# Optimization experiments

Hardware: AMD Instinct MI355X
Metric: run time of the kernel (lower is better)

The kernel has to match this reference:

```python
import jax, jax.numpy as jnp
import numpy as np

D_MODEL = 768
STATE_N = 16
BATCH = 8
SEQ = 2048


def setup_inputs() -> dict:
    key = jax.random.key(0)
    ks = jax.random.split(key, 12)
    d, n = D_MODEL, STATE_N
    s = 0.02
    inp = {
        "x": jax.random.normal(ks[0], (BATCH, SEQ, d), dtype=jnp.float32),
        # A_log init as in module: log(arange(1..N)) repeated over d_model
        "A_log": jnp.log(jnp.tile(jnp.arange(1, n + 1, dtype=jnp.float32)[None, :], (d, 1))),
        "D_param": jnp.ones((d,), dtype=jnp.float32),
        "B_proj_w": jax.random.normal(ks[1], (n, d), dtype=jnp.float32) * s,
        "C_proj_w": jax.random.normal(ks[2], (n, d), dtype=jnp.float32) * s,
        "delta_w": jax.random.normal(ks[3], (d, d), dtype=jnp.float32) * s,
        "delta_b": jax.random.normal(ks[4], (d,), dtype=jnp.float32) * s,
        "in_w": jax.random.normal(ks[5], (2 * d, d), dtype=jnp.float32) * s,
        "in_b": jax.random.normal(ks[6], (2 * d,), dtype=jnp.float32) * s,
        "out_w": jax.random.normal(ks[7], (d, d), dtype=jnp.float32) * s,
        "out_b": jax.random.normal(ks[8], (d,), dtype=jnp.float32) * s,
        "conv_w": jax.random.normal(ks[9], (d, 1, 3), dtype=jnp.float32) * s,  # depthwise [D,1,K]
        "conv_b": jax.random.normal(ks[10], (d,), dtype=jnp.float32) * s,
    }
    return inp


def _forward(x, A_log, D_param, B_proj_w, C_proj_w, delta_w, delta_b,
             in_w, in_b, out_w, out_b, conv_w, conv_b):
    A = -jnp.exp(A_log)  # [D, N]
    xz = jnp.einsum("bld,ed->ble", x, in_w) + in_b  # [B, L, 2D]
    x_in, z = jnp.split(xz, 2, axis=-1)
    # depthwise conv1d, padding=1, groups=D (cross-correlation, same as torch)
    x_c = jax.lax.conv_general_dilated(
        jnp.transpose(x_in, (0, 2, 1)), conv_w,
        window_strides=(1,), padding=((1, 1),),
        feature_group_count=x.shape[-1],
        dimension_numbers=("NCH", "OIH", "NCH"))
    x_conv = jnp.transpose(x_c, (0, 2, 1)) + conv_b  # [B, L, D]
    x_conv = jax.nn.silu(x_conv)
    delta = jax.nn.softplus(jnp.einsum("bld,ed->ble", x_conv, delta_w) + delta_b)  # [B,L,D]
    B_sel = jnp.einsum("bld,nd->bln", x_conv, B_proj_w)  # [B, L, N]
    C_sel = jnp.einsum("bld,nd->bln", x_conv, C_proj_w)  # [B, L, N]

    Bsz, L, D = x.shape
    N = A.shape[1]

    def step(h, t_in):
        dt, b_t, c_t, x_t = t_in  # [B,D], [B,N], [B,N], [B,D]
        A_bar = jnp.exp(dt[:, :, None] * A[None, :, :])           # [B,D,N]
        h = A_bar * h + (dt[:, :, None] * b_t[:, None, :]) * x_t[:, :, None]
        y_t = jnp.sum(h * c_t[:, None, :], axis=-1)               # [B,D]
        return h, y_t

    xs = (jnp.transpose(delta, (1, 0, 2)), jnp.transpose(B_sel, (1, 0, 2)),
          jnp.transpose(C_sel, (1, 0, 2)), jnp.transpose(x_conv, (1, 0, 2)))
    h0 = jnp.zeros((Bsz, D, N), dtype=x.dtype)
    _, ys = jax.lax.scan(step, h0, xs)
    y = jnp.transpose(ys, (1, 0, 2))  # [B, L, D]

    y = y + x_conv * D_param[None, None, :]
    y = y * jax.nn.silu(z)
    return jnp.einsum("bld,ed->ble", y, out_w) + out_b


def reference(x, A_log, D_param, B_proj_w, C_proj_w, delta_w, delta_b,
              in_w, in_b, out_w, out_b, conv_w, conv_b):
    return _forward(x, A_log, D_param, B_proj_w, C_proj_w, delta_w, delta_b,
                    in_w, in_b, out_w, out_b, conv_w, conv_b)
```

## Files before the change

### kernel.cpp

```cpp
#include <hip/hip_runtime.h>
#include <hip/hip_bf16.h>

#define D_MODEL 768
#define SEQL    2048
#define BATCH   8
#define NSTATE  16
#define NCHUNK  32
#define TCHUNK  64

typedef __attribute__((ext_vector_type(8))) short short8;
typedef __attribute__((ext_vector_type(4))) float f32x4;

typedef const __attribute__((address_space(1))) unsigned int gas1_t;
typedef __attribute__((address_space(3))) unsigned int las3_t;

__device__ __forceinline__ void gload_lds16(const void* g, void* l) {
  __builtin_amdgcn_global_load_lds((gas1_t*)g, (las3_t*)l, 16, 0, 0);
}

__device__ __forceinline__ float b2f(short s) {
  return __uint_as_float(((unsigned)(unsigned short)s) << 16);
}
__device__ __forceinline__ short f2b(float f) {
  __hip_bfloat16 h = __float2bfloat16(f);
  return *reinterpret_cast<short*>(&h);
}

__device__ __forceinline__ unsigned tix(int r, int k) {
  return (unsigned)((((r >> 7) * 24 + (k >> 5)) << 13) + ((r & 127) << 6) +
                    ((((k >> 3) ^ ((r >> 1) & 3)) & 3) << 4) + ((k & 7) << 1));
}

__device__ __forceinline__ short8 pack8(const float* v) {
  short8 o;
#pragma unroll
  for (int e = 0; e < 8; ++e) o[e] = f2b(v[e]);
  return o;
}

__global__ __launch_bounds__(256) void prep_all(
    const float* __restrict__ x, const float* __restrict__ in_w,
    const float* __restrict__ delta_w, const float* __restrict__ Bp,
    const float* __restrict__ Cp, const float* __restrict__ out_w,
    const float* __restrict__ A_log,
    char* __restrict__ xb, char* __restrict__ w_in,
    char* __restrict__ w_dbc, char* __restrict__ w_out,
    float* __restrict__ A2) {
  int i = blockIdx.x * 256 + threadIdx.x;
  if (i < 16384 * 96) {
    const int r = i / 96, k8 = i - r * 96;
    float v[8];
    *(float4*)(v) = *(const float4*)(x + (size_t)r * 768 + k8 * 8);
    *(float4*)(v + 4) = *(const float4*)(x + (size_t)r * 768 + k8 * 8 + 4);
    *(short8*)(xb + tix(r, k8 * 8)) = pack8(v);
    return;
  }
  i -= 16384 * 96;
  if (i < 1536 * 96) {
    const int r = i / 96, k8 = i - r * 96;
    float v[8];
    *(float4*)(v) = *(const float4*)(in_w + (size_t)r * 768 + k8 * 8);
    *(float4*)(v + 4) = *(const float4*)(in_w + (size_t)r * 768 + k8 * 8 + 4);
    *(short8*)(w_in + tix(r, k8 * 8)) = pack8(v);
    return;
  }
  i -= 1536 * 96;
  if (i < 896 * 96) {
    const int r = i / 96, k8 = i - r * 96;
    float v[8];
    const float* src = (r < 768)   ? delta_w + (size_t)r * 768
                       : (r < 784) ? Bp + (size_t)(r - 768) * 768
                       : (r < 800) ? Cp + (size_t)(r - 784) * 768
                                   : nullptr;
    if (src) {
      *(float4*)(v) = *(const float4*)(src + k8 * 8);
      *(float4*)(v + 4) = *(const float4*)(src + k8 * 8 + 4);
    } else {
#pragma unroll
      for (int e = 0; e < 8; ++e) v[e] = 0.f;
    }
    *(short8*)(w_dbc + tix(r, k8 * 8)) = pack8(v);
    return;
  }
  i -= 896 * 96;
  if (i < 768 * 96) {
    const int r = i / 96, k8 = i - r * 96;
    float v[8];
    *(float4*)(v) = *(const float4*)(out_w + (size_t)r * 768 + k8 * 8);
    *(float4*)(v + 4) = *(const float4*)(out_w + (size_t)r * 768 + k8 * 8 + 4);
    *(short8*)(w_out + tix(r, k8 * 8)) = pack8(v);
    return;
  }
  i -= 768 * 96;
  A2[i] = -expf(A_log[i]) * 1.44269504088896f;
}

template <int MODE>
__global__ __launch_bounds__(256, 3) void gemm128tb(
    const char* __restrict__ Amat, const char* __restrict__ Bw,
    const float* __restrict__ bias, void* __restrict__ out0,
    void* __restrict__ out1, void* __restrict__ out2, const int gxn) {
  constexpr int KT = 24;
  __shared__ char lds[49152];
  const int tid  = threadIdx.x;
  const int lane = tid & 63, wave = tid >> 6;
  const int wr = wave >> 1, wc = wave & 1;

  const int nwg = gridDim.x, id = blockIdx.x;
  const int swz = (id & 7) * (nwg >> 3) + (id >> 3);
  const int tm = swz / gxn, tn = swz - tm * gxn;

  const char* gA = Amat + ((size_t)tm * KT) * 8192 + (tid << 4);
  const char* gB = Bw   + ((size_t)tn * KT) * 8192 + (tid << 4);
  const int ldst = tid << 4;

  const int frow = lane & 15, fq = lane >> 4;
  const int pc = (fq << 4) ^ (((frow >> 1) & 3) << 4);
  const int aoff = ((wr * 64 + frow) << 6) + pc;
  const int boff = ((wc * 64 + frow) << 6) + pc;

  f32x4 acc[4][4];
#pragma unroll
  for (int m = 0; m < 4; ++m)
#pragma unroll
    for (int n = 0; n < 4; ++n) acc[m][n] = (f32x4){0.f, 0.f, 0.f, 0.f};

#define STAGE(buf, kt)                                                          \
  {                                                                             \
    const char* sA = gA + (kt) * 8192;                                          \
    const char* sB = gB + (kt) * 8192;                                          \
    char* dA = lds + (buf) * 16384 + ldst;                                      \
    char* dB = dA + 8192;                                                       \
    gload_lds16(sA, dA);                                                        \
    gload_lds16(sA + 4096, dA + 4096);                                          \
    gload_lds16(sB, dB);                                                        \
    gload_lds16(sB + 4096, dB + 4096);                                          \
  }
#define VMW(n) asm volatile("s_waitcnt vmcnt(" #n ")" ::: "memory")
#define BAR    __builtin_amdgcn_s_barrier()

  STAGE(0, 0);
  STAGE(1, 1);
  VMW(4);
  BAR;

  int bc = 0;
  for (int kt = 0; kt < KT; ++kt) {
    short8 a[4], b[4];
    const char* ba = lds + bc * 16384;
#pragma unroll
    for (int m = 0; m < 4; ++m) a[m] = *(const short8*)(ba + aoff + m * 1024);
#pragma unroll
    for (int n = 0; n < 4; ++n) b[n] = *(const short8*)(ba + 8192 + boff + n * 1024);
    const bool st = (kt + 2 < KT);
    if (st) {
      const int b2 = bc + 2 >= 3 ? bc - 1 : bc + 2;
      STAGE(b2, kt + 2);
    }
    __builtin_amdgcn_s_setprio(1);
#pragma unroll
    for (int m = 0; m < 4; ++m)
#pragma unroll
      for (int n = 0; n < 4; ++n)
        acc[m][n] = __builtin_amdgcn_mfma_f32_16x16x32_bf16(a[m], b[n], acc[m][n], 0, 0, 0);
    __builtin_amdgcn_s_setprio(0);
    if (st)                VMW(4);
    else if (kt + 2 == KT) VMW(0);
    BAR;
    bc = bc + 1 >= 3 ? 0 : bc + 1;
  }

  const int rowA0 = tm * 128, rowB0 = tn * 128;
#pragma unroll
  for (int m = 0; m < 4; ++m) {
    const int grow0 = rowA0 + wr * 64 + m * 16 + fq * 4;
#pragma unroll
    for (int n = 0; n < 4; ++n) {
      const int gcol = rowB0 + wc * 64 + n * 16 + frow;
#pragma unroll
      for (int i = 0; i < 4; ++i) {
        const int grow = grow0 + i;
        float v = acc[m][n][i];
        if (MODE == 0) {
          v += bias[gcol];
          if (gcol < 768)
            *(short*)((char*)out0 + tix(grow, gcol)) = f2b(v);
          else
            *(short*)((char*)out1 + tix(grow, gcol - 768)) = f2b(v);
        } else if (MODE == 1) {
          if (gcol < 768) {
            v += bias[gcol];
            float sp = (v > 20.f) ? v : log1pf(expf(v));
            *(short*)((char*)out0 + tix(grow, gcol)) = f2b(sp);
          } else if (gcol < 784) {
            ((float*)out1)[(size_t)grow * 16 + (gcol - 768)] = v;
          } else if (gcol < 800) {
            ((float*)out2)[(size_t)grow * 16 + (gcol - 784)] = v;
          }
        } else {
          ((float*)out0)[(size_t)grow * 768 + gcol] = v + bias[gcol];
        }
      }
    }
  }
#undef STAGE
#undef VMW
#undef BAR
}

__global__ __launch_bounds__(256) void conv_silu8(
    const char* __restrict__ xin, const float* __restrict__ conv_w,
    const float* __restrict__ conv_b, char* __restrict__ xc) {
  const int idx = blockIdx.x * 256 + threadIdx.x;
  const int r  = idx / 96;
  const int d8 = (idx - r * 96) * 8;
  const int t  = r & (SEQL - 1);

  short8 x0 = *(const short8*)(xin + tix(r, d8));
  short8 xm = {}, xp = {};
  if (t > 0)        xm = *(const short8*)(xin + tix(r - 1, d8));
  if (t < SEQL - 1) xp = *(const short8*)(xin + tix(r + 1, d8));

  const float4* cw4 = (const float4*)(conv_w + d8 * 3);
  float4 cw[6];
#pragma unroll
  for (int q = 0; q < 6; ++q) cw[q] = cw4[q];
  float4 cb0 = *(const float4*)(conv_b + d8);
  float4 cb1 = *(const float4*)(conv_b + d8 + 4);
  const float* cwf = (const float*)cw;
  const float* cbf0 = (const float*)&cb0;
  const float* cbf1 = (const float*)&cb1;

  short8 res;
#pragma unroll
  for (int e = 0; e < 8; ++e) {
    float acc = (e < 4) ? cbf0[e] : cbf1[e - 4];
    acc = fmaf(cwf[e * 3 + 0], b2f(xm[e]), acc);
    acc = fmaf(cwf[e * 3 + 1], b2f(x0[e]), acc);
    acc = fmaf(cwf[e * 3 + 2], b2f(xp[e]), acc);
    const float sig = 1.f / (1.f + __expf(-acc));
    res[e] = f2b(acc * sig);
  }
  *(short8*)(xc + tix(r, d8)) = res;
}

__global__ __launch_bounds__(256) void scan_pass1(
    const char* __restrict__ delta, const char* __restrict__ xconv,
    const float* __restrict__ Bsel, const float* __restrict__ A2,
    float* __restrict__ sumdt, float* __restrict__ Sbuf) {
  const int d = blockIdx.x * 256 + threadIdx.x;
  const int b = blockIdx.y, c = blockIdx.z;
  __shared__ float sB[TCHUNK * 16];
  ((float4*)sB)[threadIdx.x] =
      ((const float4*)(Bsel + ((size_t)b * SEQL + c * TCHUNK) * 16))[threadIdx.x];
  __syncthreads();

  float a2[16];
#pragma unroll
  for (int n = 0; n < 16; ++n) a2[n] = A2[d * 16 + n];
  float h[16] = {};
  float sdt = 0.f;
  const int r0 = b * SEQL + c * TCHUNK;
  const unsigned tb = (((unsigned)((r0 >> 7) * 24 + (d >> 5))) << 13) + ((r0 & 127) << 6);
  const unsigned sd0 = (d >> 3) & 3;
  const unsigned klo = (d & 7) << 1;
  for (int t = 0; t < TCHUNK; ++t) {
    const unsigned ro = tb + t * 64 + (((sd0 ^ ((unsigned)t >> 1)) & 3) << 4) + klo;
    const float dt = b2f(*(const short*)(delta + ro));
    const float x = b2f(*(const short*)(xconv + ro));
    sdt += dt;
    const float dtx = dt * x;
    const float* Br = &sB[t * 16];
#pragma unroll
    for (int n = 0; n < 16; ++n) {
      const float a = exp2f(dt * a2[n]);
      h[n] = fmaf(a, h[n], dtx * Br[n]);
    }
  }
  sumdt[((size_t)b * NCHUNK + c) * 768 + d] = sdt;
#pragma unroll
  for (int n = 0; n < 16; ++n)
    Sbuf[(((size_t)b * NCHUNK + c) * 16 + n) * 768 + d] = h[n];
}

__global__ __launch_bounds__(256) void scan_carry(
    const float* __restrict__ sumdt, const float* __restrict__ Sbuf,
    const float* __restrict__ A2, float* __restrict__ Hin) {
  const int idx = blockIdx.x * 256 + threadIdx.x;
  const int d = idx % 768;
  const int n = (idx / 768) & 15;
  const int b = idx / (768 * 16);
  const float a2 = A2[d * 16 + n];
  float h = 0.f;
  for (int c = 0; c < NCHUNK; ++c) {
    const size_t hb = (((size_t)(b * NCHUNK + c)) * 16 + n) * 768 + d;
    Hin[hb] = h;
    const float sd = sumdt[(b * NCHUNK + c) * 768 + d];
    h = fmaf(exp2f(sd * a2), h, Sbuf[hb]);
  }
}

__global__ __launch_bounds__(256) void scan_pass3(
    const char* __restrict__ delta, const char* __restrict__ xconv,
    const char* __restrict__ zb, const float* __restrict__ Bsel,
    const float* __restrict__ Csel, const float* __restrict__ A2,
    const float* __restrict__ Hin, const float* __restrict__ Dp,
    char* __restrict__ yg) {
  const int d = blockIdx.x * 256 + threadIdx.x;
  const int b = blockIdx.y, c = blockIdx.z;
  __shared__ float sB[TCHUNK * 16], sC[TCHUNK * 16];
  {
    const size_t off = ((size_t)b * SEQL + c * TCHUNK) * 16;
    ((float4*)sB)[threadIdx.x] = ((const float4*)(Bsel + off))[threadIdx.x];
    ((float4*)sC)[threadIdx.x] = ((const float4*)(Csel + off))[threadIdx.x];
  }
  __syncthreads();

  float a2[16];
#pragma unroll
  for (int n = 0; n < 16; ++n) a2[n] = A2[d * 16 + n];
  float h[16];
  {
    const size_t hb = ((size_t)b * NCHUNK + c) * 16 * 768 + d;
#pragma unroll
    for (int n = 0; n < 16; ++n) h[n] = Hin[hb + (size_t)n * 768];
  }
  const float Dpd = Dp[d];
  const int r0 = b * SEQL + c * TCHUNK;
  const unsigned tb = (((unsigned)((r0 >> 7) * 24 + (d >> 5))) << 13) + ((r0 & 127) << 6);
  const unsigned sd0 = (d >> 3) & 3;
  const unsigned klo = (d & 7) << 1;
  for (int t = 0; t < TCHUNK; ++t) {
    const unsigned ro = tb + t * 64 + (((sd0 ^ ((unsigned)t >> 1)) & 3) << 4) + klo;
    const float dt = b2f(*(const short*)(delta + ro));
    const float x = b2f(*(const short*)(xconv + ro));
    const float dtx = dt * x;
    const float* Br = &sB[t * 16];
    const float* Cr = &sC[t * 16];
    float y = 0.f;
#pragma unroll
    for (int n = 0; n < 16; ++n) {
      const float a = exp2f(dt * a2[n]);
      h[n] = fmaf(a, h[n], dtx * Br[n]);
      y = fmaf(h[n], Cr[n], y);
    }
    const float z = b2f(*(const short*)(zb + ro));
    const float sig = 1.f / (1.f + __expf(-z));
    const float out = (y + x * Dpd) * (z * sig);
    *(short*)(yg + ro) = f2b(out);
  }
}

extern "C" void kernel_launch(void* const* d_in, const int* in_sizes, int n_in,
                              void* d_out, int out_size, void* d_ws, size_t ws_size,
                              hipStream_t stream) {
  const float* x       = (const float*)d_in[0];
  const float* A_log   = (const float*)d_in[1];
  const float* D_param = (const float*)d_in[2];
  const float* B_proj  = (const float*)d_in[3];
  const float* C_proj  = (const float*)d_in[4];
  const float* delta_w = (const float*)d_in[5];
  const float* delta_b = (const float*)d_in[6];
  const float* in_w    = (const float*)d_in[7];
  const float* in_b    = (const float*)d_in[8];
  const float* out_w   = (const float*)d_in[9];
  const float* out_b   = (const float*)d_in[10];
  const float* conv_w  = (const float*)d_in[11];
  const float* conv_b  = (const float*)d_in[12];

  char* ws = (char*)d_ws;
  char*  xb       = ws + 0;
  char*  w_in_b   = ws + 25165824;
  char*  w_dbc_b  = ws + 27525120;
  char*  w_out_b  = ws + 28901376;
  float* A2       = (float*)(ws + 30081024);
  char*  xin_b    = ws + 30130176;
  char*  z_b      = ws + 55296000;
  char*  xconv_b  = ws + 80461824;
  char*  delta_bf = ws + 105627648;
  float* Bsel     = (float*)(ws + 130793472);
  float* Csel     = (float*)(ws + 131842048);
  float* sumdt    = (float*)(ws + 132890624);
  float* Sbuf     = (float*)(ws + 133677056);
  float* Hin      = (float*)(ws + 146259968);
  char*  yg       = xb;

  prep_all<<<7392, 256, 0, stream>>>(x, in_w, delta_w, B_proj, C_proj, out_w, A_log,
                                     xb, w_in_b, w_dbc_b, w_out_b, A2);
  gemm128tb<0><<<1536, 256, 0, stream>>>(xb, w_in_b, in_b, xin_b, z_b, nullptr, 12);
  conv_silu8<<<16384 * 96 / 256, 256, 0, stream>>>(xin_b, conv_w, conv_b, xconv_b);
  gemm128tb<1><<<896, 256, 0, stream>>>(xconv_b, w_dbc_b, delta_b, delta_bf, Bsel, Csel, 7);
  scan_pass1<<<dim3(3, BATCH, NCHUNK), 256, 0, stream>>>(delta_bf, xconv_b, Bsel, A2, sumdt, Sbuf);
  scan_carry<<<384, 256, 0, stream>>>(sumdt, Sbuf, A2, Hin);
  scan_pass3<<<dim3(3, BATCH, NCHUNK), 256, 0, stream>>>(delta_bf, xconv_b, z_b, Bsel, Csel, A2,
                                                         Hin, D_param, yg);
  gemm128tb<2><<<768, 256, 0, stream>>>(yg, w_out_b, out_b, (float*)d_out, nullptr, nullptr, 6);
}
```

Measured before the change: 355.6 us.

## Replace LDS-staged GEMM pipeline with direct global-to-register double-buffered loads

The three GEMMs stop staging tiles through LDS via global_load_lds with a triple buffer. Each wave now loads its MFMA fragments straight from global memory into registers, double-buffered across k-steps. This removes the LDS traffic and the vmcnt waits. In exchange, each block reads A and B tiles redundantly per wave (each wave row/col pair re-fetches the same data), so global/L2 traffic rises. Register pressure also increases, and the launch-bounds occupancy hint of 3 is dropped.

After: 353.3 us. No clear change (-0.6%).

```diff
diff --git a/kernel.cpp b/kernel.cpp
--- a/kernel.cpp
+++ b/kernel.cpp
@@ -10,13 +10,6 @@
 
 typedef __attribute__((ext_vector_type(8))) short short8;
 typedef __attribute__((ext_vector_type(4))) float f32x4;
-
-typedef const __attribute__((address_space(1))) unsigned int gas1_t;
-typedef __attribute__((address_space(3))) unsigned int las3_t;
-
-__device__ __forceinline__ void gload_lds16(const void* g, void* l) {
-  __builtin_amdgcn_global_load_lds((gas1_t*)g, (las3_t*)l, 16, 0, 0);
-}
 
 __device__ __forceinline__ float b2f(short s) {
   return __uint_as_float(((unsigned)(unsigned short)s) << 16);
@@ -96,12 +89,10 @@
 }
 
 template <int MODE>
-__global__ __launch_bounds__(256, 3) void gemm128tb(
+__global__ __launch_bounds__(256) void gemm128r(
     const char* __restrict__ Amat, const char* __restrict__ Bw,
     const float* __restrict__ bias, void* __restrict__ out0,
     void* __restrict__ out1, void* __restrict__ out2, const int gxn) {
-  constexpr int KT = 24;
-  __shared__ char lds[49152];
   const int tid  = threadIdx.x;
   const int lane = tid & 63, wave = tid >> 6;
   const int wr = wave >> 1, wc = wave & 1;
@@ -109,65 +100,49 @@
   const int nwg = gridDim.x, id = blockIdx.x;
   const int swz = (id & 7) * (nwg >> 3) + (id >> 3);
   const int tm = swz / gxn, tn = swz - tm * gxn;
-
-  const char* gA = Amat + ((size_t)tm * KT) * 8192 + (tid << 4);
-  const char* gB = Bw   + ((size_t)tn * KT) * 8192 + (tid << 4);
-  const int ldst = tid << 4;
 
   const int frow = lane & 15, fq = lane >> 4;
   const int pc = (fq << 4) ^ (((frow >> 1) & 3) << 4);
   const int aoff = ((wr * 64 + frow) << 6) + pc;
   const int boff = ((wc * 64 + frow) << 6) + pc;
 
+  const char* Ab = Amat + (size_t)(tm * 24) * 8192 + aoff;
+  const char* Bb = Bw   + (size_t)(tn * 24) * 8192 + boff;
+
   f32x4 acc[4][4];
 #pragma unroll
   for (int m = 0; m < 4; ++m)
 #pragma unroll
     for (int n = 0; n < 4; ++n) acc[m][n] = (f32x4){0.f, 0.f, 0.f, 0.f};
 
-#define STAGE(buf, kt)                                                          \
+  short8 a0[4], b0[4], a1[4], b1[4];
+#define LOADF(A, B, kt)                                                         \
   {                                                                             \
-    const char* sA = gA + (kt) * 8192;                                          \
-    const char* sB = gB + (kt) * 8192;                                          \
-    char* dA = lds + (buf) * 16384 + ldst;                                      \
-    char* dB = dA + 8192;                                                       \
-    gload_lds16(sA, dA);                                                        \
-    gload_lds16(sA + 4096, dA + 4096);                                          \
-    gload_lds16(sB, dB);                                                        \
-    gload_lds16(sB + 4096, dB + 4096);                                          \
-  }
-#define VMW(n) asm volatile("s_waitcnt vmcnt(" #n ")" ::: "memory")
-#define BAR    __builtin_amdgcn_s_barrier()
-
-  STAGE(0, 0);
-  STAGE(1, 1);
-  VMW(4);
-  BAR;
-
-  int bc = 0;
-  for (int kt = 0; kt < KT; ++kt) {
-    short8 a[4], b[4];
-    const char* ba = lds + bc * 16384;
-#pragma unroll
-    for (int m = 0; m < 4; ++m) a[m] = *(const short8*)(ba + aoff + m * 1024);
-#pragma unroll
-    for (int n = 0; n < 4; ++n) b[n] = *(const short8*)(ba + 8192 + boff + n * 1024);
-    const bool st = (kt + 2 < KT);
-    if (st) {
-      const int b2 = bc + 2 >= 3 ? bc - 1 : bc + 2;
-      STAGE(b2, kt + 2);
-    }
-    __builtin_amdgcn_s_setprio(1);
-#pragma unroll
-    for (int m = 0; m < 4; ++m)
-#pragma unroll
-      for (int n = 0; n < 4; ++n)
-        acc[m][n] = __builtin_amdgcn_mfma_f32_16x16x32_bf16(a[m], b[n], acc[m][n], 0, 0, 0);
-    __builtin_amdgcn_s_setprio(0);
-    if (st)                VMW(4);
-    else if (kt + 2 == KT) VMW(0);
-    BAR;
-    bc = bc + 1 >= 3 ? 0 : bc + 1;
+    const char* pa = Ab + (kt) * 8192;                                          \
+    const char* pb = Bb + (kt) * 8192;                                          \
+    _Pragma("unroll") for (int m = 0; m < 4; ++m)                               \
+        A[m] = *(const short8*)(pa + m * 1024);                                 \
+    _Pragma("unroll") for (int n = 0; n < 4; ++n)                               \
+        B[n] = *(const short8*)(pb + n * 1024);                                 \
+  }
+#define MMA(A, B)                                                               \
+  {                                                                             \
+    __builtin_amdgcn_s_setprio(1);                                              \
+    _Pragma("unroll") for (int m = 0; m < 4; ++m)                               \
+    _Pragma("unroll") for (int n = 0; n < 4; ++n)                               \
+        acc[m][n] = __builtin_amdgcn_mfma_f32_16x16x32_bf16(A[m], B[n],         \
+                                                            acc[m][n], 0, 0, 0);\
+    __builtin_amdgcn_s_setprio(0);                                              \
+  }
+
+  LOADF(a0, b0, 0);
+  for (int kt = 0; kt < 24; kt += 2) {
+    LOADF(a1, b1, kt + 1);
+    __builtin_amdgcn_s_barrier();
+    MMA(a0, b0);
+    if (kt + 2 < 24) LOADF(a0, b0, kt + 2);
+    __builtin_amdgcn_s_barrier();
+    MMA(a1, b1);
   }
 
   const int rowA0 = tm * 128, rowB0 = tn * 128;
@@ -203,9 +178,8 @@
       }
     }
   }
-#undef STAGE
-#undef VMW
-#undef BAR
+#undef LOADF
+#undef MMA
 }
 
 __global__ __launch_bounds__(256) void conv_silu8(
@@ -387,12 +361,12 @@
 
   prep_all<<<7392, 256, 0, stream>>>(x, in_w, delta_w, B_proj, C_proj, out_w, A_log,
                                      xb, w_in_b, w_dbc_b, w_out_b, A2);
-  gemm128tb<0><<<1536, 256, 0, stream>>>(xb, w_in_b, in_b, xin_b, z_b, nullptr, 12);
+  gemm128r<0><<<1536, 256, 0, stream>>>(xb, w_in_b, in_b, xin_b, z_b, nullptr, 12);
   conv_silu8<<<16384 * 96 / 256, 256, 0, stream>>>(xin_b, conv_w, conv_b, xconv_b);
-  gemm128tb<1><<<896, 256, 0, stream>>>(xconv_b, w_dbc_b, delta_b, delta_bf, Bsel, Csel, 7);
+  gemm128r<1><<<896, 256, 0, stream>>>(xconv_b, w_dbc_b, delta_b, delta_bf, Bsel, Csel, 7);
   scan_pass1<<<dim3(3, BATCH, NCHUNK), 256, 0, stream>>>(delta_bf, xconv_b, Bsel, A2, sumdt, Sbuf);
   scan_carry<<<384, 256, 0, stream>>>(sumdt, Sbuf, A2, Hin);
   scan_pass3<<<dim3(3, BATCH, NCHUNK), 256, 0, stream>>>(delta_bf, xconv_b, z_b, Bsel, Csel, A2,
                                                          Hin, D_param, yg);
-  gemm128tb<2><<<768, 256, 0, stream>>>(yg, w_out_b, out_b, (float*)d_out, nullptr, nullptr, 6);
-}
+  gemm128r<2><<<768, 256, 0, stream>>>(yg, w_out_b, out_b, (float*)d_out, nullptr, nullptr, 6);
+}
```
